# Kernel tuning notes

Measured on AMD Instinct MI355X. Metric: run time of the kernel, lower is better.

Reference implementation:

```python
import jax, jax.numpy as jnp
import numpy as np

LN_EPS = 1e-5
NORM_EPS = 1e-12
TEMPERATURE = 0.5


def _project(h, W1, b1, W2, b2, g, beta):
    # projection head: Linear -> ReLU -> Linear -> LayerNorm, then L2 normalize
    x = jnp.maximum(h @ W1 + b1, 0.0) @ W2 + b2          # [B, P]
    mu = jnp.mean(x, axis=-1, keepdims=True)
    var = jnp.mean(jnp.square(x - mu), axis=-1, keepdims=True)
    x = (x - mu) * jax.lax.rsqrt(var + LN_EPS) * g + beta
    n = jnp.linalg.norm(x, axis=-1, keepdims=True)
    return x / jnp.maximum(n, NORM_EPS)                   # [B, P]


def setup_inputs() -> dict:
    key = jax.random.key(0)
    ks = jax.random.split(key, 8)
    B, H, P, K, NBUF = 16384, 2048, 256, 64, 2000
    Hh = H // 2
    return {
        "hidden_states": jax.random.normal(ks[0], (B, H), jnp.float32),
        "positive_hidden": jax.random.normal(ks[1], (B, H), jnp.float32),
        "neg_buffer": jax.random.normal(ks[2], (NBUF, P), jnp.float32),
        "W1": jax.random.normal(ks[3], (H, Hh), jnp.float32) * (1.0 / np.sqrt(H)),
        "b1": jnp.zeros((Hh,), jnp.float32),
        "W2": jax.random.normal(ks[4], (Hh, P), jnp.float32) * (1.0 / np.sqrt(Hh)),
        "b2": jnp.zeros((P,), jnp.float32),
        "ln_gamma": jnp.ones((P,), jnp.float32),
        "ln_beta": jnp.zeros((P,), jnp.float32),
        "neg_indices": jax.random.randint(ks[5], (B, K), 0, NBUF, jnp.int32),
    }


def reference(hidden_states, positive_hidden, neg_buffer, W1, b1, W2, b2,
              ln_gamma, ln_beta, neg_indices):
    anchors = _project(hidden_states, W1, b1, W2, b2, ln_gamma, ln_beta)      # [B,P]
    positives = _project(positive_hidden, W1, b1, W2, b2, ln_gamma, ln_beta)  # [B,P]
    # negatives are detached in the original (buffer stores .detach() features)
    negs = jax.lax.stop_gradient(neg_buffer)[neg_indices]                      # [B,K,P]
    pos_sim = jnp.einsum('bp,bp->b', anchors, positives) / TEMPERATURE        # [B]
    neg_sims = jnp.einsum('bkp,bp->bk', negs, anchors) / TEMPERATURE          # [B,K]
    logits = jnp.concatenate([pos_sim[:, None], neg_sims], axis=1)            # [B,1+K]
    # cross-entropy with label 0 for every anchor, averaged over the batch
    loss = -jnp.mean(jax.nn.log_softmax(logits, axis=-1)[:, 0])
    return loss
```

## Files before the change

kernel.cpp:

```cpp
#include <hip/hip_runtime.h>
#include <hip/hip_bf16.h>
#include <cstdint>

#define BATCH   16384
#define HDIM    2048
#define HHDIM   1024
#define PDIM    256
#define KNEG    64
#define NBUF    2000
#define M1      (2 * BATCH)

typedef float  f32x4  __attribute__((ext_vector_type(4)));
typedef __bf16 bf16x8 __attribute__((ext_vector_type(8)));

typedef __attribute__((address_space(3))) unsigned int       lds_u32;
typedef __attribute__((address_space(1))) const unsigned int glb_u32;

__device__ __forceinline__ void gload_lds16(const void* g, void* l) {
  __builtin_amdgcn_global_load_lds((glb_u32*)g, (lds_u32*)l, 16, 0, 0);
}

__device__ __forceinline__ float dot4(f32x4 a, f32x4 b) {
  return a[0]*b[0] + a[1]*b[1] + a[2]*b[2] + a[3]*b[3];
}

#define VMCNT(n) asm volatile("s_waitcnt vmcnt(" #n ")" ::: "memory")
#define LGKM(n)  asm volatile("s_waitcnt lgkmcnt(" #n ")" ::: "memory")

__global__ __launch_bounds__(256)
void cast_bf16_kernel(const float* __restrict__ src, __bf16* __restrict__ dst,
                      long n8) {
  long i = (long)blockIdx.x * blockDim.x + threadIdx.x;
  long stride = (long)gridDim.x * blockDim.x;
  for (; i < n8; i += stride) {
    f32x4 a = ((const f32x4*)src)[2 * i];
    f32x4 b = ((const f32x4*)src)[2 * i + 1];
    bf16x8 w;
    for (int j = 0; j < 4; ++j) { w[j] = (__bf16)a[j]; w[4 + j] = (__bf16)b[j]; }
    ((bf16x8*)dst)[i] = w;
  }
}

__global__ void transpose_cast_kernel(const float* __restrict__ src,
                                      __bf16* __restrict__ dst, int K, int N) {
  __shared__ float tile[32][33];
  int bn = blockIdx.x * 32, bk = blockIdx.y * 32;
  int tx = threadIdx.x, ty = threadIdx.y;
  for (int j = 0; j < 32; j += 8)
    tile[ty + j][tx] = src[(size_t)(bk + ty + j) * N + bn + tx];
  __syncthreads();
  for (int j = 0; j < 32; j += 8)
    dst[(size_t)(bn + ty + j) * K + bk + tx] = (__bf16)tile[tx][ty + j];
}

template <int KD, int BMH, int NBt, bool RELU_OUT, int GRID>
__global__ __launch_bounds__(512)
void gemm_8ph(const __bf16* __restrict__ A, const __bf16* __restrict__ Bt,
              const float* __restrict__ bias, void* __restrict__ Cv) {
  constexpr int KT    = KD / 64;
  constexpr int MI    = BMH / 32;
  constexpr int AHALF = BMH * 64;
  constexpr int BHALF = 128 * 64;
  constexpr int ASTEP = 2 * AHALF;
  constexpr int BSTEP = 2 * BHALF;
  constexpr int NDIM  = NBt * 256;
  constexpr int AUL   = BMH / 64;

  __shared__ __bf16 lA[2 * ASTEP];
  __shared__ __bf16 lB[2 * BSTEP];

  constexpr int Q = GRID / 8;
  int bid = blockIdx.x;
  int swb = (bid & 7) * Q + (bid >> 3);
  const int mb = swb / NBt, nb = swb % NBt;
  const long mrow0 = (long)mb * (2 * BMH);
  const int  ncol0 = nb * 256;

  const int tid = threadIdx.x;
  const int wid = tid >> 6, lane = tid & 63;
  const int wr = wid >> 2, wc = wid & 3;
  const int fl = lane & 15, fh = lane >> 4;

  int aoff[MI][2], boff[2][2];
  #pragma unroll
  for (int mi = 0; mi < MI; ++mi)
    #pragma unroll
    for (int ks = 0; ks < 2; ++ks) {
      int row = wr * (BMH / 2) + mi * 16 + fl;
      aoff[mi][ks] = row * 64 + (((ks * 4 + fh) ^ (row & 7)) * 8);
    }
  #pragma unroll
  for (int ni = 0; ni < 2; ++ni)
    #pragma unroll
    for (int ks = 0; ks < 2; ++ks) {
      int row = wc * 32 + ni * 16 + fl;
      boff[ni][ks] = row * 64 + (((ks * 4 + fh) ^ (row & 7)) * 8);
    }

  const int r0 = tid >> 3, sl = tid & 7;
  long aS[2][AUL], bS[2][2];
  #pragma unroll
  for (int h = 0; h < 2; ++h) {
    #pragma unroll
    for (int i = 0; i < AUL; ++i) {
      int rr = r0 + i * 64;
      int ss = sl ^ (rr & 7);
      aS[h][i] = (mrow0 + h * BMH + rr) * (long)KD + ss * 8;
    }
    #pragma unroll
    for (int i = 0; i < 2; ++i) {
      int rr = r0 + i * 64;
      int ss = sl ^ (rr & 7);
      bS[h][i] = ((long)(ncol0 + h * 128 + rr)) * KD + ss * 8;
    }
  }
  const int dstw = wid * 512;

  auto stA = [&](int h, int t) {
    __bf16* base = lA + (t & 1) * ASTEP + h * AHALF + dstw;
    #pragma unroll
    for (int i = 0; i < AUL; ++i)
      gload_lds16(A + aS[h][i] + (long)t * 64, (void*)(base + i * 4096));
  };
  auto stB = [&](int h, int t) {
    __bf16* base = lB + (t & 1) * BSTEP + h * BHALF + dstw;
    #pragma unroll
    for (int i = 0; i < 2; ++i)
      gload_lds16(Bt + bS[h][i] + (long)t * 64, (void*)(base + i * 4096));
  };

  bf16x8 areg[MI][2], breg0[2][2], breg1[2][2];
  auto loadA = [&](int mh, int s) {
    const __bf16* base = lA + (s & 1) * ASTEP + mh * AHALF;
    #pragma unroll
    for (int mi = 0; mi < MI; ++mi)
      #pragma unroll
      for (int ks = 0; ks < 2; ++ks)
        areg[mi][ks] = *(const bf16x8*)(base + aoff[mi][ks]);
  };
  auto loadB = [&](bf16x8 (&br)[2][2], int nh, int s) {
    const __bf16* base = lB + (s & 1) * BSTEP + nh * BHALF;
    #pragma unroll
    for (int ni = 0; ni < 2; ++ni)
      #pragma unroll
      for (int ks = 0; ks < 2; ++ks)
        br[ni][ks] = *(const bf16x8*)(base + boff[ni][ks]);
  };

  f32x4 acc[2][2][MI][2] = {};

#define PHASE_MFMA(mh, nh, BR)                                                \
  __builtin_amdgcn_s_setprio(1);                                              \
  _Pragma("unroll")                                                           \
  for (int ks = 0; ks < 2; ++ks) {                                            \
    _Pragma("unroll")                                                         \
    for (int mi = 0; mi < MI; ++mi) {                                         \
      _Pragma("unroll")                                                       \
      for (int ni = 0; ni < 2; ++ni)                                          \
        acc[mh][nh][mi][ni] = __builtin_amdgcn_mfma_f32_16x16x32_bf16(        \
            areg[mi][ks], BR[ni][ks], acc[mh][nh][mi][ni], 0, 0, 0);          \
    }                                                                         \
  }                                                                           \
  __builtin_amdgcn_s_setprio(0);

  stA(0, 0); stB(0, 0); stA(1, 0); stB(1, 0);
  stA(0, 1); stB(1, 1); stB(0, 1); stA(1, 1);
  if constexpr (BMH == 128) { VMCNT(8); } else { VMCNT(6); }
  __builtin_amdgcn_s_barrier();
  __builtin_amdgcn_sched_barrier(0);

  for (int s = 0; s < KT; ++s) {
    loadA(0, s);
    loadB(breg0, 0, s);
    if (s >= 1 && s + 1 < KT) stB(0, s + 1);
    if constexpr (BMH == 128) LGKM(8);
    __builtin_amdgcn_s_barrier();
    LGKM(0);
    __builtin_amdgcn_sched_barrier(0);
    PHASE_MFMA(0, 0, breg0);
    __builtin_amdgcn_s_barrier();

    loadB(breg1, 1, s);
    if (s >= 1 && s + 1 < KT) stA(1, s + 1);
    __builtin_amdgcn_s_barrier();
    LGKM(0);
    __builtin_amdgcn_sched_barrier(0);
    PHASE_MFMA(0, 1, breg1);
    __builtin_amdgcn_s_barrier();

    loadA(1, s);
    if (s + 2 < KT) stA(0, s + 2);
    __builtin_amdgcn_s_barrier();
    LGKM(0);
    __builtin_amdgcn_sched_barrier(0);
    PHASE_MFMA(1, 1, breg1);
    __builtin_amdgcn_s_barrier();

    if (s + 2 < KT) stB(1, s + 2);
    __builtin_amdgcn_s_barrier();
    __builtin_amdgcn_sched_barrier(0);
    PHASE_MFMA(1, 0, breg0);
    if (s + 2 < KT) {
      if constexpr (BMH == 128) { VMCNT(4); } else { VMCNT(3); }
    } else {
      VMCNT(0);
    }
    __builtin_amdgcn_s_barrier();
    __builtin_amdgcn_sched_barrier(0);
  }

#undef PHASE_MFMA

  #pragma unroll
  for (int mh = 0; mh < 2; ++mh)
    #pragma unroll
    for (int nh = 0; nh < 2; ++nh)
      #pragma unroll
      for (int ni = 0; ni < 2; ++ni) {
        int col = ncol0 + nh * 128 + wc * 32 + ni * 16 + fl;
        float bv = bias[col];
        #pragma unroll
        for (int mi = 0; mi < MI; ++mi)
          #pragma unroll
          for (int r = 0; r < 4; ++r) {
            long row = mrow0 + mh * BMH + wr * (BMH / 2) + mi * 16 + fh * 4 + r;
            float v = acc[mh][nh][mi][ni][r] + bv;
            if constexpr (RELU_OUT) {
              v = fmaxf(v, 0.0f);
              ((__bf16*)Cv)[row * NDIM + col] = (__bf16)v;
            } else {
              ((float*)Cv)[row * NDIM + col] = v;
            }
          }
      }
}

__device__ __forceinline__ int swz(int row) { return (row >> 1) & 3; }

template <int KD, int NB, bool AF32, bool RELU_OUT>
__global__ __launch_bounds__(256)
void gemm_mfma(const void* __restrict__ A0v, const void* __restrict__ A1v,
               const __bf16* __restrict__ Bt, const float* __restrict__ bias,
               void* __restrict__ Cv) {
  __shared__ __bf16 lA[128 * 32];
  __shared__ __bf16 lB[128 * 32];

  const int total_wg = (M1 / 128) * NB;
  int bid = blockIdx.x;
  const int q = total_wg >> 3;
  int swzb = (bid & 7) * q + (bid >> 3);
  const int mb = swzb / NB, nb = swzb % NB;
  const int mrow0 = mb * 128, ncol0 = nb * 128;
  const int NDIM = NB * 128;

  const int tid = threadIdx.x;
  const int wid = tid >> 6, lane = tid & 63;
  const int wr = wid >> 1, wc = wid & 1;
  const int fl = lane & 15, fh = lane >> 4;

  const float*  Af = nullptr;
  const __bf16* Ab = nullptr;
  if constexpr (AF32) {
    const float* A0 = (const float*)A0v;
    const float* A1 = (const float*)A1v;
    Af = (mrow0 < BATCH) ? (A0 + (size_t)mrow0 * KD)
                         : (A1 + (size_t)(mrow0 - BATCH) * KD);
  } else {
    Ab = (const __bf16*)A0v + (size_t)mrow0 * KD;
  }

  f32x4 acc[4][4] = {};
  const int a_row  = wid * 32 + (lane >> 2);
  const int a_slot = lane & 3;

  const int KT = KD / 32;
  for (int kt = 0; kt < KT; ++kt) {
    f32x4 av[2][2];
    if constexpr (AF32) {
      const float* ap = Af + (size_t)a_row * KD + kt * 32 + a_slot * 8;
      av[0][0] = *(const f32x4*)(ap);
      av[0][1] = *(const f32x4*)(ap + 4);
      av[1][0] = *(const f32x4*)(ap + (size_t)16 * KD);
      av[1][1] = *(const f32x4*)(ap + (size_t)16 * KD + 4);
    }
    __syncthreads();
    {
      int chunk = wid * 2;
      for (int c = 0; c < 2; ++c, ++chunk) {
        int row = chunk * 16 + (lane >> 2);
        int sslot = (lane & 3) ^ swz(row);
        const __bf16* srcp = Bt + (size_t)(ncol0 + row) * KD + kt * 32 + sslot * 8;
        gload_lds16(srcp, (void*)(lB + chunk * 512));
      }
    }
    if constexpr (AF32) {
      for (int r = 0; r < 2; ++r) {
        int row = a_row + r * 16;
        int sslot = a_slot ^ swz(row);
        bf16x8 w;
        for (int j = 0; j < 4; ++j) {
          w[j]     = (__bf16)av[r][0][j];
          w[4 + j] = (__bf16)av[r][1][j];
        }
        *(bf16x8*)(lA + row * 32 + sslot * 8) = w;
      }
    } else {
      int chunk = wid * 2;
      for (int c = 0; c < 2; ++c, ++chunk) {
        int row = chunk * 16 + (lane >> 2);
        int sslot = (lane & 3) ^ swz(row);
        const __bf16* srcp = Ab + (size_t)row * KD + kt * 32 + sslot * 8;
        gload_lds16(srcp, (void*)(lA + chunk * 512));
      }
    }
    __syncthreads();

    bf16x8 afr[4], bfr[4];
    for (int mi = 0; mi < 4; ++mi) {
      int row = wr * 64 + mi * 16 + fl;
      afr[mi] = *(const bf16x8*)(lA + row * 32 + (fh ^ swz(row)) * 8);
    }
    for (int ni = 0; ni < 4; ++ni) {
      int row = wc * 64 + ni * 16 + fl;
      bfr[ni] = *(const bf16x8*)(lB + row * 32 + (fh ^ swz(row)) * 8);
    }
    for (int mi = 0; mi < 4; ++mi)
      for (int ni = 0; ni < 4; ++ni)
        acc[mi][ni] = __builtin_amdgcn_mfma_f32_16x16x32_bf16(
            afr[mi], bfr[ni], acc[mi][ni], 0, 0, 0);
  }

  for (int ni = 0; ni < 4; ++ni) {
    int col = ncol0 + wc * 64 + ni * 16 + fl;
    float bv = bias[col];
    for (int mi = 0; mi < 4; ++mi) {
      for (int r = 0; r < 4; ++r) {
        size_t row = (size_t)mrow0 + wr * 64 + mi * 16 + fh * 4 + r;
        float v = acc[mi][ni][r] + bv;
        if constexpr (RELU_OUT) {
          v = fmaxf(v, 0.0f);
          ((__bf16*)Cv)[row * NDIM + col] = (__bf16)v;
        } else {
          ((float*)Cv)[row * NDIM + col] = v;
        }
      }
    }
  }
}

__global__ __launch_bounds__(256)
void ln_l2_kernel(float* __restrict__ X, const float* __restrict__ g,
                  const float* __restrict__ be) {
  int row  = blockIdx.x * 4 + (threadIdx.x >> 6);
  int lane = threadIdx.x & 63;
  float* xp = X + (size_t)row * PDIM + lane * 4;
  f32x4 v = *(const f32x4*)xp;

  float s = v[0] + v[1] + v[2] + v[3];
  for (int m = 1; m < 64; m <<= 1) s += __shfl_xor(s, m, 64);
  float mu = s * (1.0f / PDIM);

  f32x4 d;
  for (int j = 0; j < 4; ++j) d[j] = v[j] - mu;
  float qv = dot4(d, d);
  for (int m = 1; m < 64; m <<= 1) qv += __shfl_xor(qv, m, 64);
  float rs = rsqrtf(qv * (1.0f / PDIM) + 1e-5f);

  f32x4 g4 = *(const f32x4*)(g + lane * 4);
  f32x4 b4 = *(const f32x4*)(be + lane * 4);
  f32x4 y;
  for (int j = 0; j < 4; ++j) y[j] = d[j] * rs * g4[j] + b4[j];

  float n2 = dot4(y, y);
  for (int m = 1; m < 64; m <<= 1) n2 += __shfl_xor(n2, m, 64);
  float sc = 1.0f / fmaxf(sqrtf(n2), 1e-12f);
  for (int j = 0; j < 4; ++j) y[j] *= sc;
  *(f32x4*)xp = y;
}

__global__ __launch_bounds__(256)
void loss_kernel(const float* __restrict__ X, const float* __restrict__ negbuf,
                 const int* __restrict__ nidx, float* __restrict__ partials) {
  __shared__ float lsum[4];
  int b    = blockIdx.x * 4 + (threadIdx.x >> 6);
  int lane = threadIdx.x & 63;
  int g = lane >> 4, lg = lane & 15;

  const float* arow = X + (size_t)b * PDIM;
  const float* prow = X + (size_t)(BATCH + b) * PDIM;

  f32x4 a4[4];
  for (int j = 0; j < 4; ++j) a4[j] = *(const f32x4*)(arow + lg * 16 + j * 4);

  float ps = 0.0f;
  for (int j = 0; j < 4; ++j) {
    f32x4 p = *(const f32x4*)(prow + lg * 16 + j * 4);
    ps += dot4(a4[j], p);
  }
  for (int m = 1; m < 16; m <<= 1) ps += __shfl_xor(ps, m, 64);
  float pos = ps * 2.0f;

  float myneg = -3.0e38f;
  for (int k4 = 0; k4 < 16; ++k4) {
    int k = k4 * 4 + g;
    int idx = nidx[(size_t)b * KNEG + k];
    const float* nrow = negbuf + (size_t)idx * PDIM;
    float sv = 0.0f;
    for (int j = 0; j < 4; ++j) {
      f32x4 nv = *(const f32x4*)(nrow + lg * 16 + j * 4);
      sv += dot4(a4[j], nv);
    }
    for (int m = 1; m < 16; m <<= 1) sv += __shfl_xor(sv, m, 64);
    if (lg == k4) myneg = sv * 2.0f;
  }

  float mx = myneg;
  for (int m = 1; m < 64; m <<= 1) mx = fmaxf(mx, __shfl_xor(mx, m, 64));
  mx = fmaxf(mx, pos);
  float e = expf(myneg - mx);
  for (int m = 1; m < 64; m <<= 1) e += __shfl_xor(e, m, 64);
  float tot = e + expf(pos - mx);
  float lb = -(pos - mx - logf(tot));

  if (lane == 0) lsum[threadIdx.x >> 6] = lb;
  __syncthreads();
  if (threadIdx.x == 0)
    partials[blockIdx.x] = lsum[0] + lsum[1] + lsum[2] + lsum[3];
}

__global__ void finalize_kernel(const float* __restrict__ partials,
                                float* __restrict__ out) {
  __shared__ float ls[4];
  int tid = threadIdx.x;
  float s = 0.0f;
  for (int i = tid; i < 4096; i += 256) s += partials[i];
  for (int m = 1; m < 64; m <<= 1) s += __shfl_xor(s, m, 64);
  if ((tid & 63) == 0) ls[tid >> 6] = s;
  __syncthreads();
  if (tid == 0) out[0] = (ls[0] + ls[1] + ls[2] + ls[3]) * (1.0f / BATCH);
}

extern "C" void kernel_launch(void* const* d_in, const int* in_sizes, int n_in,
                              void* d_out, int out_size, void* d_ws, size_t ws_size,
                              hipStream_t stream) {
  const float* hidden   = (const float*)d_in[0];
  const float* positive = (const float*)d_in[1];
  const float* negbuf   = (const float*)d_in[2];
  const float* W1       = (const float*)d_in[3];
  const float* b1       = (const float*)d_in[4];
  const float* W2       = (const float*)d_in[5];
  const float* b2       = (const float*)d_in[6];
  const float* gamma    = (const float*)d_in[7];
  const float* beta     = (const float*)d_in[8];
  const int*   nidx     = (const int*)d_in[9];
  float* out = (float*)d_out;

  char* ws = (char*)d_ws;

  const size_t OFF_Y1   = 134217728;
  const size_t OFF_W1T  = OFF_Y1 + 67108864;
  const size_t OFF_W2T  = OFF_W1T + 4194304;
  const size_t OFF_PART = OFF_W2T + 524288;
  const size_t NEED_BIG = OFF_PART + 16384;

  const bool big = (ws_size >= NEED_BIG);

  __bf16* W1T; __bf16* W2T; __bf16* Y1; float* X; float* partials;
  __bf16* Abf = nullptr;
  if (big) {
    Abf      = (__bf16*)(ws);
    Y1       = (__bf16*)(ws + OFF_Y1);
    W1T      = (__bf16*)(ws + OFF_W1T);
    W2T      = (__bf16*)(ws + OFF_W2T);
    partials = (float*) (ws + OFF_PART);
    X        = (float*) (ws);
  } else {
    W1T      = (__bf16*)(ws);
    W2T      = (__bf16*)(ws + 4194304);
    Y1       = (__bf16*)(ws + 4718592);
    X        = (float*) (ws + 71827456);
    partials = (float*) (ws + 105381888);
  }

  transpose_cast_kernel<<<dim3(HHDIM / 32, HDIM / 32), dim3(32, 8), 0, stream>>>(
      W1, W1T, HDIM, HHDIM);
  transpose_cast_kernel<<<dim3(PDIM / 32, HHDIM / 32), dim3(32, 8), 0, stream>>>(
      W2, W2T, HHDIM, PDIM);

  if (big) {
    const long n8 = (long)BATCH * HDIM / 8;
    cast_bf16_kernel<<<2048, 256, 0, stream>>>(hidden, Abf, n8);
    cast_bf16_kernel<<<2048, 256, 0, stream>>>(positive, Abf + (size_t)BATCH * HDIM, n8);

    gemm_8ph<HDIM, 128, HHDIM / 256, true, (M1 / 256) * (HHDIM / 256)>
        <<<(M1 / 256) * (HHDIM / 256), 512, 0, stream>>>(Abf, W1T, b1, Y1);

    gemm_8ph<HHDIM, 64, PDIM / 256, false, (M1 / 128) * (PDIM / 256)>
        <<<(M1 / 128) * (PDIM / 256), 512, 0, stream>>>(Y1, W2T, b2, X);
  } else {
    gemm_mfma<HDIM, HHDIM / 128, true, true>
        <<<(M1 / 128) * (HHDIM / 128), 256, 0, stream>>>(
            hidden, positive, W1T, b1, Y1);
    gemm_mfma<HHDIM, PDIM / 128, false, false>
        <<<(M1 / 128) * (PDIM / 128), 256, 0, stream>>>(
            Y1, nullptr, W2T, b2, X);
  }

  ln_l2_kernel<<<M1 / 4, 256, 0, stream>>>(X, gamma, beta);
  loss_kernel<<<BATCH / 4, 256, 0, stream>>>(X, negbuf, nidx, partials);
  finalize_kernel<<<1, 256, 0, stream>>>(partials, out);
}
```

Baseline: 339.4 us.

## Fuse fp32-to-bf16 cast into GEMM1 loads and LayerNorm/L2 into GEMM2 epilogue

```diff
diff --git a/kernel.cpp b/kernel.cpp
--- a/kernel.cpp
+++ b/kernel.cpp
@@ -26,20 +26,6 @@
 
 #define VMCNT(n) asm volatile("s_waitcnt vmcnt(" #n ")" ::: "memory")
 #define LGKM(n)  asm volatile("s_waitcnt lgkmcnt(" #n ")" ::: "memory")
-
-__global__ __launch_bounds__(256)
-void cast_bf16_kernel(const float* __restrict__ src, __bf16* __restrict__ dst,
-                      long n8) {
-  long i = (long)blockIdx.x * blockDim.x + threadIdx.x;
-  long stride = (long)gridDim.x * blockDim.x;
-  for (; i < n8; i += stride) {
-    f32x4 a = ((const f32x4*)src)[2 * i];
-    f32x4 b = ((const f32x4*)src)[2 * i + 1];
-    bf16x8 w;
-    for (int j = 0; j < 4; ++j) { w[j] = (__bf16)a[j]; w[4 + j] = (__bf16)b[j]; }
-    ((bf16x8*)dst)[i] = w;
-  }
-}
 
 __global__ void transpose_cast_kernel(const float* __restrict__ src,
                                       __bf16* __restrict__ dst, int K, int N) {
@@ -53,10 +39,13 @@
     dst[(size_t)(bn + ty + j) * K + bk + tx] = (__bf16)tile[tx][ty + j];
 }
 
-template <int KD, int BMH, int NBt, bool RELU_OUT, int GRID>
+template <int KD, int BMH, int NBt, bool AF32, bool RELU_OUT, bool LNFUSE, int GRID>
 __global__ __launch_bounds__(512)
-void gemm_8ph(const __bf16* __restrict__ A, const __bf16* __restrict__ Bt,
-              const float* __restrict__ bias, void* __restrict__ Cv) {
+void gemm_8ph(const void* __restrict__ A0v, const void* __restrict__ A1v,
+              const __bf16* __restrict__ Bt, const float* __restrict__ bias,
+              const float* __restrict__ lng, const float* __restrict__ lnb,
+              void* __restrict__ Cv) {
+  static_assert(!LNFUSE || NBt == 1, "LN fusion needs full rows per block");
   constexpr int KT    = KD / 64;
   constexpr int MI    = BMH / 32;
   constexpr int AHALF = BMH * 64;
@@ -98,35 +87,69 @@
     }
 
   const int r0 = tid >> 3, sl = tid & 7;
-  long aS[2][AUL], bS[2][2];
+  long bS[2][2];
   #pragma unroll
-  for (int h = 0; h < 2; ++h) {
-    #pragma unroll
-    for (int i = 0; i < AUL; ++i) {
-      int rr = r0 + i * 64;
-      int ss = sl ^ (rr & 7);
-      aS[h][i] = (mrow0 + h * BMH + rr) * (long)KD + ss * 8;
-    }
+  for (int h = 0; h < 2; ++h)
     #pragma unroll
     for (int i = 0; i < 2; ++i) {
       int rr = r0 + i * 64;
       int ss = sl ^ (rr & 7);
       bS[h][i] = ((long)(ncol0 + h * 128 + rr)) * KD + ss * 8;
     }
-  }
   const int dstw = wid * 512;
+
+  auto stB = [&](int h, int t) {
+    __bf16* base = lB + (t & 1) * BSTEP + h * BHALF + dstw;
+    #pragma unroll
+    for (int i = 0; i < 2; ++i)
+      gload_lds16(Bt + bS[h][i] + (long)t * 64, (void*)(base + i * 4096));
+  };
+
+  long aS[2][AUL];
+  const float* Afp = nullptr;
+  if constexpr (AF32) {
+    const float* A0 = (const float*)A0v;
+    const float* A1 = (const float*)A1v;
+    Afp = (mrow0 < BATCH) ? (A0 + (size_t)mrow0 * KD)
+                          : (A1 + (size_t)(mrow0 - BATCH) * KD);
+  } else {
+    #pragma unroll
+    for (int h = 0; h < 2; ++h)
+      #pragma unroll
+      for (int i = 0; i < AUL; ++i) {
+        int rr = r0 + i * 64;
+        int ss = sl ^ (rr & 7);
+        aS[h][i] = (mrow0 + h * BMH + rr) * (long)KD + ss * 8;
+      }
+  }
 
   auto stA = [&](int h, int t) {
     __bf16* base = lA + (t & 1) * ASTEP + h * AHALF + dstw;
     #pragma unroll
     for (int i = 0; i < AUL; ++i)
-      gload_lds16(A + aS[h][i] + (long)t * 64, (void*)(base + i * 4096));
-  };
-  auto stB = [&](int h, int t) {
-    __bf16* base = lB + (t & 1) * BSTEP + h * BHALF + dstw;
-    #pragma unroll
-    for (int i = 0; i < 2; ++i)
-      gload_lds16(Bt + bS[h][i] + (long)t * 64, (void*)(base + i * 4096));
+      gload_lds16((const __bf16*)A0v + aS[h][i] + (long)t * 64,
+                  (void*)(base + i * 4096));
+  };
+
+  const int rowA = tid >> 2, pA = tid & 3;
+  f32x4 aq[4];
+  auto issueA = [&](int h, int t) {
+    const float* p = Afp + (size_t)(h * 128 + rowA) * KD + t * 64 + pA * 16;
+    aq[0] = *(const f32x4*)(p);
+    aq[1] = *(const f32x4*)(p + 4);
+    aq[2] = *(const f32x4*)(p + 8);
+    aq[3] = *(const f32x4*)(p + 12);
+  };
+  auto writeA = [&](int h, int t) {
+    bf16x8 w0, w1;
+    #pragma unroll
+    for (int j = 0; j < 4; ++j) {
+      w0[j] = (__bf16)aq[0][j]; w0[4 + j] = (__bf16)aq[1][j];
+      w1[j] = (__bf16)aq[2][j]; w1[4 + j] = (__bf16)aq[3][j];
+    }
+    __bf16* base = lA + (t & 1) * ASTEP + h * AHALF + rowA * 64;
+    *(bf16x8*)(base + (((2 * pA)     ^ (rowA & 7)) * 8)) = w0;
+    *(bf16x8*)(base + (((2 * pA + 1) ^ (rowA & 7)) * 8)) = w1;
   };
 
   bf16x8 areg[MI][2], breg0[2][2], breg1[2][2];
@@ -163,15 +186,25 @@
   }                                                                           \
   __builtin_amdgcn_s_setprio(0);
 
-  stA(0, 0); stB(0, 0); stA(1, 0); stB(1, 0);
-  stA(0, 1); stB(1, 1); stB(0, 1); stA(1, 1);
-  if constexpr (BMH == 128) { VMCNT(8); } else { VMCNT(6); }
+  if constexpr (AF32) {
+    issueA(0, 0); writeA(0, 0);
+    issueA(1, 0); writeA(1, 0);
+    issueA(0, 1); writeA(0, 1);
+    issueA(1, 1); writeA(1, 1);
+  } else {
+    stA(0, 0); stA(1, 0); stA(0, 1); stA(1, 1);
+  }
+  stB(0, 0); stB(1, 0); stB(0, 1); stB(1, 1);
+  if constexpr (AF32)           { VMCNT(4); LGKM(0); }
+  else if constexpr (BMH == 128){ VMCNT(8); }
+  else                          { VMCNT(6); }
   __builtin_amdgcn_s_barrier();
   __builtin_amdgcn_sched_barrier(0);
 
   for (int s = 0; s < KT; ++s) {
     loadA(0, s);
     loadB(breg0, 0, s);
+    if constexpr (AF32) { if (s >= 1 && s + 1 < KT) issueA(1, s + 1); }
     if (s >= 1 && s + 1 < KT) stB(0, s + 1);
     if constexpr (BMH == 128) LGKM(8);
     __builtin_amdgcn_s_barrier();
@@ -181,7 +214,8 @@
     __builtin_amdgcn_s_barrier();
 
     loadB(breg1, 1, s);
-    if (s >= 1 && s + 1 < KT) stA(1, s + 1);
+    if constexpr (AF32) { if (s >= 1 && s + 1 < KT) writeA(1, s + 1); }
+    else                { if (s >= 1 && s + 1 < KT) stA(1, s + 1); }
     __builtin_amdgcn_s_barrier();
     LGKM(0);
     __builtin_amdgcn_sched_barrier(0);
@@ -189,19 +223,24 @@
     __builtin_amdgcn_s_barrier();
 
     loadA(1, s);
-    if (s + 2 < KT) stA(0, s + 2);
+    if constexpr (AF32) { if (s + 2 < KT) issueA(0, s + 2); }
+    else                { if (s + 2 < KT) stA(0, s + 2); }
     __builtin_amdgcn_s_barrier();
     LGKM(0);
     __builtin_amdgcn_sched_barrier(0);
     PHASE_MFMA(1, 1, breg1);
     __builtin_amdgcn_s_barrier();
 
+    if constexpr (AF32) { if (s + 2 < KT) writeA(0, s + 2); }
     if (s + 2 < KT) stB(1, s + 2);
     __builtin_amdgcn_s_barrier();
+    LGKM(0);
     __builtin_amdgcn_sched_barrier(0);
     PHASE_MFMA(1, 0, breg0);
     if (s + 2 < KT) {
-      if constexpr (BMH == 128) { VMCNT(4); } else { VMCNT(3); }
+      if constexpr (AF32)            { VMCNT(2); }
+      else if constexpr (BMH == 128) { VMCNT(4); }
+      else                           { VMCNT(3); }
     } else {
       VMCNT(0);
     }
@@ -211,171 +250,132 @@
 
 #undef PHASE_MFMA
 
-  #pragma unroll
-  for (int mh = 0; mh < 2; ++mh)
+  if constexpr (LNFUSE) {
+    float (*s1p)[4] = (float(*)[4])((float*)lA);
+    float (*s2p)[4] = (float(*)[4])((float*)lA + 512);
+    float (*n2p)[4] = (float(*)[4])((float*)lA + 1024);
+
+    float v[2][2][MI][2][4];
+    float gg[2][2], bb[2][2];
     #pragma unroll
     for (int nh = 0; nh < 2; ++nh)
       #pragma unroll
       for (int ni = 0; ni < 2; ++ni) {
-        int col = ncol0 + nh * 128 + wc * 32 + ni * 16 + fl;
-        float bv = bias[col];
-        #pragma unroll
-        for (int mi = 0; mi < MI; ++mi)
+        int c = nh * 128 + wc * 32 + ni * 16 + fl;
+        float bv = bias[c];
+        gg[nh][ni] = lng[c]; bb[nh][ni] = lnb[c];
+        #pragma unroll
+        for (int mh = 0; mh < 2; ++mh)
           #pragma unroll
-          for (int r = 0; r < 4; ++r) {
-            long row = mrow0 + mh * BMH + wr * (BMH / 2) + mi * 16 + fh * 4 + r;
-            float v = acc[mh][nh][mi][ni][r] + bv;
-            if constexpr (RELU_OUT) {
-              v = fmaxf(v, 0.0f);
-              ((__bf16*)Cv)[row * NDIM + col] = (__bf16)v;
-            } else {
-              ((float*)Cv)[row * NDIM + col] = v;
+          for (int mi = 0; mi < MI; ++mi)
+            #pragma unroll
+            for (int r = 0; r < 4; ++r)
+              v[mh][nh][mi][ni][r] = acc[mh][nh][mi][ni][r] + bv;
+      }
+
+    #pragma unroll
+    for (int mh = 0; mh < 2; ++mh)
+      #pragma unroll
+      for (int mi = 0; mi < MI; ++mi)
+        #pragma unroll
+        for (int r = 0; r < 4; ++r) {
+          float s1 = 0.0f, s2 = 0.0f;
+          #pragma unroll
+          for (int nh = 0; nh < 2; ++nh)
+            #pragma unroll
+            for (int ni = 0; ni < 2; ++ni) {
+              float x = v[mh][nh][mi][ni][r];
+              s1 += x; s2 += x * x;
             }
+          for (int m = 1; m < 16; m <<= 1) {
+            s1 += __shfl_xor(s1, m, 64);
+            s2 += __shfl_xor(s2, m, 64);
           }
-      }
-}
-
-__device__ __forceinline__ int swz(int row) { return (row >> 1) & 3; }
-
-template <int KD, int NB, bool AF32, bool RELU_OUT>
-__global__ __launch_bounds__(256)
-void gemm_mfma(const void* __restrict__ A0v, const void* __restrict__ A1v,
-               const __bf16* __restrict__ Bt, const float* __restrict__ bias,
-               void* __restrict__ Cv) {
-  __shared__ __bf16 lA[128 * 32];
-  __shared__ __bf16 lB[128 * 32];
-
-  const int total_wg = (M1 / 128) * NB;
-  int bid = blockIdx.x;
-  const int q = total_wg >> 3;
-  int swzb = (bid & 7) * q + (bid >> 3);
-  const int mb = swzb / NB, nb = swzb % NB;
-  const int mrow0 = mb * 128, ncol0 = nb * 128;
-  const int NDIM = NB * 128;
-
-  const int tid = threadIdx.x;
-  const int wid = tid >> 6, lane = tid & 63;
-  const int wr = wid >> 1, wc = wid & 1;
-  const int fl = lane & 15, fh = lane >> 4;
-
-  const float*  Af = nullptr;
-  const __bf16* Ab = nullptr;
-  if constexpr (AF32) {
-    const float* A0 = (const float*)A0v;
-    const float* A1 = (const float*)A1v;
-    Af = (mrow0 < BATCH) ? (A0 + (size_t)mrow0 * KD)
-                         : (A1 + (size_t)(mrow0 - BATCH) * KD);
+          if (fl == 0) {
+            int lr = mh * 64 + wr * 32 + mi * 16 + fh * 4 + r;
+            s1p[lr][wc] = s1; s2p[lr][wc] = s2;
+          }
+        }
+    __syncthreads();
+
+    float n2loc[2][MI][4];
+    #pragma unroll
+    for (int mh = 0; mh < 2; ++mh)
+      #pragma unroll
+      for (int mi = 0; mi < MI; ++mi)
+        #pragma unroll
+        for (int r = 0; r < 4; ++r) {
+          int lr = mh * 64 + wr * 32 + mi * 16 + fh * 4 + r;
+          float t1 = s1p[lr][0] + s1p[lr][1] + s1p[lr][2] + s1p[lr][3];
+          float t2 = s2p[lr][0] + s2p[lr][1] + s2p[lr][2] + s2p[lr][3];
+          float mu = t1 * (1.0f / PDIM);
+          float var = t2 * (1.0f / PDIM) - mu * mu;
+          float rstd = rsqrtf(var + 1e-5f);
+          float n2 = 0.0f;
+          #pragma unroll
+          for (int nh = 0; nh < 2; ++nh)
+            #pragma unroll
+            for (int ni = 0; ni < 2; ++ni) {
+              float y = (v[mh][nh][mi][ni][r] - mu) * rstd * gg[nh][ni] + bb[nh][ni];
+              v[mh][nh][mi][ni][r] = y;
+              n2 += y * y;
+            }
+          for (int m = 1; m < 16; m <<= 1) n2 += __shfl_xor(n2, m, 64);
+          n2loc[mh][mi][r] = n2;
+        }
+    #pragma unroll
+    for (int mh = 0; mh < 2; ++mh)
+      #pragma unroll
+      for (int mi = 0; mi < MI; ++mi)
+        #pragma unroll
+        for (int r = 0; r < 4; ++r)
+          if (fl == 0) {
+            int lr = mh * 64 + wr * 32 + mi * 16 + fh * 4 + r;
+            n2p[lr][wc] = n2loc[mh][mi][r];
+          }
+    __syncthreads();
+
+    #pragma unroll
+    for (int mh = 0; mh < 2; ++mh)
+      #pragma unroll
+      for (int mi = 0; mi < MI; ++mi)
+        #pragma unroll
+        for (int r = 0; r < 4; ++r) {
+          int lr = mh * 64 + wr * 32 + mi * 16 + fh * 4 + r;
+          float t = n2p[lr][0] + n2p[lr][1] + n2p[lr][2] + n2p[lr][3];
+          float sc = 1.0f / fmaxf(sqrtf(t), 1e-12f);
+          #pragma unroll
+          for (int nh = 0; nh < 2; ++nh)
+            #pragma unroll
+            for (int ni = 0; ni < 2; ++ni) {
+              int c = nh * 128 + wc * 32 + ni * 16 + fl;
+              ((float*)Cv)[(mrow0 + lr) * NDIM + c] = v[mh][nh][mi][ni][r] * sc;
+            }
+        }
   } else {
-    Ab = (const __bf16*)A0v + (size_t)mrow0 * KD;
-  }
-
-  f32x4 acc[4][4] = {};
-  const int a_row  = wid * 32 + (lane >> 2);
-  const int a_slot = lane & 3;
-
-  const int KT = KD / 32;
-  for (int kt = 0; kt < KT; ++kt) {
-    f32x4 av[2][2];
-    if constexpr (AF32) {
-      const float* ap = Af + (size_t)a_row * KD + kt * 32 + a_slot * 8;
-      av[0][0] = *(const f32x4*)(ap);
-      av[0][1] = *(const f32x4*)(ap + 4);
-      av[1][0] = *(const f32x4*)(ap + (size_t)16 * KD);
-      av[1][1] = *(const f32x4*)(ap + (size_t)16 * KD + 4);
-    }
-    __syncthreads();
-    {
-      int chunk = wid * 2;
-      for (int c = 0; c < 2; ++c, ++chunk) {
-        int row = chunk * 16 + (lane >> 2);
-        int sslot = (lane & 3) ^ swz(row);
-        const __bf16* srcp = Bt + (size_t)(ncol0 + row) * KD + kt * 32 + sslot * 8;
-        gload_lds16(srcp, (void*)(lB + chunk * 512));
-      }
-    }
-    if constexpr (AF32) {
-      for (int r = 0; r < 2; ++r) {
-        int row = a_row + r * 16;
-        int sslot = a_slot ^ swz(row);
-        bf16x8 w;
-        for (int j = 0; j < 4; ++j) {
-          w[j]     = (__bf16)av[r][0][j];
-          w[4 + j] = (__bf16)av[r][1][j];
+    #pragma unroll
+    for (int mh = 0; mh < 2; ++mh)
+      #pragma unroll
+      for (int nh = 0; nh < 2; ++nh)
+        #pragma unroll
+        for (int ni = 0; ni < 2; ++ni) {
+          int col = ncol0 + nh * 128 + wc * 32 + ni * 16 + fl;
+          float bv = bias[col];
+          #pragma unroll
+          for (int mi = 0; mi < MI; ++mi)
+            #pragma unroll
+            for (int r = 0; r < 4; ++r) {
+              long row = mrow0 + mh * BMH + wr * (BMH / 2) + mi * 16 + fh * 4 + r;
+              float x = acc[mh][nh][mi][ni][r] + bv;
+              if constexpr (RELU_OUT) {
+                x = fmaxf(x, 0.0f);
+                ((__bf16*)Cv)[row * NDIM + col] = (__bf16)x;
+              } else {
+                ((float*)Cv)[row * NDIM + col] = x;
+              }
+            }
         }
-        *(bf16x8*)(lA + row * 32 + sslot * 8) = w;
-      }
-    } else {
-      int chunk = wid * 2;
-      for (int c = 0; c < 2; ++c, ++chunk) {
-        int row = chunk * 16 + (lane >> 2);
-        int sslot = (lane & 3) ^ swz(row);
-        const __bf16* srcp = Ab + (size_t)row * KD + kt * 32 + sslot * 8;
-        gload_lds16(srcp, (void*)(lA + chunk * 512));
-      }
-    }
-    __syncthreads();
-
-    bf16x8 afr[4], bfr[4];
-    for (int mi = 0; mi < 4; ++mi) {
-      int row = wr * 64 + mi * 16 + fl;
-      afr[mi] = *(const bf16x8*)(lA + row * 32 + (fh ^ swz(row)) * 8);
-    }
-    for (int ni = 0; ni < 4; ++ni) {
-      int row = wc * 64 + ni * 16 + fl;
-      bfr[ni] = *(const bf16x8*)(lB + row * 32 + (fh ^ swz(row)) * 8);
-    }
-    for (int mi = 0; mi < 4; ++mi)
-      for (int ni = 0; ni < 4; ++ni)
-        acc[mi][ni] = __builtin_amdgcn_mfma_f32_16x16x32_bf16(
-            afr[mi], bfr[ni], acc[mi][ni], 0, 0, 0);
-  }
-
-  for (int ni = 0; ni < 4; ++ni) {
-    int col = ncol0 + wc * 64 + ni * 16 + fl;
-    float bv = bias[col];
-    for (int mi = 0; mi < 4; ++mi) {
-      for (int r = 0; r < 4; ++r) {
-        size_t row = (size_t)mrow0 + wr * 64 + mi * 16 + fh * 4 + r;
-        float v = acc[mi][ni][r] + bv;
-        if constexpr (RELU_OUT) {
-          v = fmaxf(v, 0.0f);
-          ((__bf16*)Cv)[row * NDIM + col] = (__bf16)v;
-        } else {
-          ((float*)Cv)[row * NDIM + col] = v;
-        }
-      }
-    }
-  }
-}
-
-__global__ __launch_bounds__(256)
-void ln_l2_kernel(float* __restrict__ X, const float* __restrict__ g,
-                  const float* __restrict__ be) {
-  int row  = blockIdx.x * 4 + (threadIdx.x >> 6);
-  int lane = threadIdx.x & 63;
-  float* xp = X + (size_t)row * PDIM + lane * 4;
-  f32x4 v = *(const f32x4*)xp;
-
-  float s = v[0] + v[1] + v[2] + v[3];
-  for (int m = 1; m < 64; m <<= 1) s += __shfl_xor(s, m, 64);
-  float mu = s * (1.0f / PDIM);
-
-  f32x4 d;
-  for (int j = 0; j < 4; ++j) d[j] = v[j] - mu;
-  float qv = dot4(d, d);
-  for (int m = 1; m < 64; m <<= 1) qv += __shfl_xor(qv, m, 64);
-  float rs = rsqrtf(qv * (1.0f / PDIM) + 1e-5f);
-
-  f32x4 g4 = *(const f32x4*)(g + lane * 4);
-  f32x4 b4 = *(const f32x4*)(be + lane * 4);
-  f32x4 y;
-  for (int j = 0; j < 4; ++j) y[j] = d[j] * rs * g4[j] + b4[j];
-
-  float n2 = dot4(y, y);
-  for (int m = 1; m < 64; m <<= 1) n2 += __shfl_xor(n2, m, 64);
-  float sc = 1.0f / fmaxf(sqrtf(n2), 1e-12f);
-  for (int j = 0; j < 4; ++j) y[j] *= sc;
-  *(f32x4*)xp = y;
+  }
 }
 
 __global__ __launch_bounds__(256)
@@ -456,57 +456,25 @@
   float* out = (float*)d_out;
 
   char* ws = (char*)d_ws;
-
-  const size_t OFF_Y1   = 134217728;
-  const size_t OFF_W1T  = OFF_Y1 + 67108864;
-  const size_t OFF_W2T  = OFF_W1T + 4194304;
-  const size_t OFF_PART = OFF_W2T + 524288;
-  const size_t NEED_BIG = OFF_PART + 16384;
-
-  const bool big = (ws_size >= NEED_BIG);
-
-  __bf16* W1T; __bf16* W2T; __bf16* Y1; float* X; float* partials;
-  __bf16* Abf = nullptr;
-  if (big) {
-    Abf      = (__bf16*)(ws);
-    Y1       = (__bf16*)(ws + OFF_Y1);
-    W1T      = (__bf16*)(ws + OFF_W1T);
-    W2T      = (__bf16*)(ws + OFF_W2T);
-    partials = (float*) (ws + OFF_PART);
-    X        = (float*) (ws);
-  } else {
-    W1T      = (__bf16*)(ws);
-    W2T      = (__bf16*)(ws + 4194304);
-    Y1       = (__bf16*)(ws + 4718592);
-    X        = (float*) (ws + 71827456);
-    partials = (float*) (ws + 105381888);
-  }
+  __bf16* W1T      = (__bf16*)(ws);
+  __bf16* W2T      = (__bf16*)(ws + 4194304);
+  __bf16* Y1       = (__bf16*)(ws + 4718592);
+  float*  X        = (float*) (ws + 71827456);
+  float*  partials = (float*) (ws + 105381888);
 
   transpose_cast_kernel<<<dim3(HHDIM / 32, HDIM / 32), dim3(32, 8), 0, stream>>>(
       W1, W1T, HDIM, HHDIM);
   transpose_cast_kernel<<<dim3(PDIM / 32, HHDIM / 32), dim3(32, 8), 0, stream>>>(
       W2, W2T, HHDIM, PDIM);
 
-  if (big) {
-    const long n8 = (long)BATCH * HDIM / 8;
-    cast_bf16_kernel<<<2048, 256, 0, stream>>>(hidden, Abf, n8);
-    cast_bf16_kernel<<<2048, 256, 0, stream>>>(positive, Abf + (size_t)BATCH * HDIM, n8);
-
-    gemm_8ph<HDIM, 128, HHDIM / 256, true, (M1 / 256) * (HHDIM / 256)>
-        <<<(M1 / 256) * (HHDIM / 256), 512, 0, stream>>>(Abf, W1T, b1, Y1);
-
-    gemm_8ph<HHDIM, 64, PDIM / 256, false, (M1 / 128) * (PDIM / 256)>
-        <<<(M1 / 128) * (PDIM / 256), 512, 0, stream>>>(Y1, W2T, b2, X);
-  } else {
-    gemm_mfma<HDIM, HHDIM / 128, true, true>
-        <<<(M1 / 128) * (HHDIM / 128), 256, 0, stream>>>(
-            hidden, positive, W1T, b1, Y1);
-    gemm_mfma<HHDIM, PDIM / 128, false, false>
-        <<<(M1 / 128) * (PDIM / 128), 256, 0, stream>>>(
-            Y1, nullptr, W2T, b2, X);
-  }
-
-  ln_l2_kernel<<<M1 / 4, 256, 0, stream>>>(X, gamma, beta);
+  gemm_8ph<HDIM, 128, HHDIM / 256, true, true, false, (M1 / 256) * (HHDIM / 256)>
+      <<<(M1 / 256) * (HHDIM / 256), 512, 0, stream>>>(
+          hidden, positive, W1T, b1, nullptr, nullptr, Y1);
+
+  gemm_8ph<HHDIM, 64, PDIM / 256, false, false, true, (M1 / 128) * (PDIM / 256)>
+      <<<(M1 / 128) * (PDIM / 256), 512, 0, stream>>>(
+          Y1, nullptr, W2T, b2, gamma, beta, X);
+
   loss_kernel<<<BATCH / 4, 256, 0, stream>>>(X, negbuf, nidx, partials);
   finalize_kernel<<<1, 256, 0, stream>>>(partials, out);
 }
```

New measurement: 334.4 us. About the same (-1.5%).
